# Kernel optimization log

Hardware: AMD Instinct MI355X
Metric: run time of the kernel (lower is better)

The kernel has to match this reference:

```python
import jax, jax.numpy as jnp
import numpy as np

WEIGHT = 1.0

# 3x3x3 discrete Laplacian stencil (6-connected, center -6), as in the torch module
_LAP_K = jnp.array(
    [[[0, 0, 0], [0, 1, 0], [0, 0, 0]],
     [[0, 1, 0], [1, -6, 1], [0, 1, 0]],
     [[0, 0, 0], [0, 1, 0], [0, 0, 0]]], dtype=jnp.float32)


def _abs_laplacian3d(x):
    """x: (N, D, H, W) -> |3D Laplacian(x)| with zero padding, same shape."""
    y = jax.lax.conv_general_dilated(
        x[:, None],              # (N, 1, D, H, W)
        _LAP_K[None, None],      # (1, 1, 3, 3, 3)
        window_strides=(1, 1, 1),
        padding=[(1, 1), (1, 1), (1, 1)])
    return jnp.abs(y[:, 0])


def setup_inputs() -> dict:
    key = jax.random.key(0)
    k1, k2 = jax.random.split(key)
    B, C, D, H, W = 2, 4, 64, 256, 256
    logits = jax.random.normal(k1, (B, C, D, H, W), dtype=jnp.float32)
    targets = jax.random.randint(k2, (B, D, H, W), 0, C)
    return {"logits": logits, "targets": targets}


def reference(logits, targets):
    B, C, D, H, W = logits.shape
    # softmax over class dim, drop background class 0 -> (B, C-1, D, H, W)
    probs = jax.nn.softmax(logits, axis=1)[:, 1:]
    # one-hot target masks for classes 1..C-1 -> (B, C-1, D, H, W)
    cls = jnp.arange(1, C)[None, :, None, None, None]
    tmask = (targets[:, None] == cls).astype(logits.dtype)
    # fused 3D Laplacian + abs over all (batch, class) pairs at once
    pred_b = _abs_laplacian3d(probs.reshape(B * (C - 1), D, H, W))
    targ_b = _abs_laplacian3d(tmask.reshape(B * (C - 1), D, H, W))
    # sum over classes of per-class MSE, divided by (C-1) == mean over everything
    return WEIGHT * jnp.mean((pred_b - targ_b) ** 2)
```

## Files before the change

### kernel.cpp

```cpp
#include <hip/hip_runtime.h>


#define CS   (1 << 22)
#define NTOT_INV (1.0f / 25165824.0f)
#define BIAS3 ((8 << 20) | (8 << 10) | 8)
#define BAR() asm volatile("s_waitcnt lgkmcnt(0)\n\ts_barrier" ::: "memory")

#define ISSUE(S, off)                                                        \
    S##0 = *(const float4*)(L + lBase + (off));                              \
    S##1 = *(const float4*)(L + lBase + (off) + CS);                         \
    S##2 = *(const float4*)(L + lBase + (off) + 2 * CS);                     \
    S##3 = *(const float4*)(L + lBase + (off) + 3 * CS);                     \
    S##t = *(const int4*)(T + tBase + (off));

__device__ __forceinline__ void smax1(float x0, float x1, float x2, float x3,
                                      float vm, float& p1, float& p2, float& p3) {
    float m  = fmaxf(fmaxf(x0, x1), fmaxf(x2, x3));
    float e0 = __expf(x0 - m);
    float e1 = __expf(x1 - m);
    float e2 = __expf(x2 - m);
    float e3 = __expf(x3 - m);
    float r  = vm * __builtin_amdgcn_rcpf(e0 + e1 + e2 + e3);
    p1 = e1 * r; p2 = e2 * r; p3 = e3 * r;
}

__device__ __forceinline__ int ohenc(int t, int msk) {
    int nz = (t > 0) ? 1 : 0;
    return (nz << (((t - 1) & 3) * 10)) & msk;
}

__global__ __launch_bounds__(512) void boundary_loss_kernel(
        const float* __restrict__ L,
        const int*   __restrict__ T,
        float*       __restrict__ out) {
    const int tid  = threadIdx.x;
    const int lane = tid & 63;
    const int th   = tid >> 6;
    int bi = blockIdx.x;
    const int dseg = bi & 7;  bi >>= 3;
    const int ht   = bi % 43;
    const int b    = bi / 43;

    const int   h   = ht * 6 + th - 1;
    const bool  hv  = ((unsigned)h < 256u);
    const int   hcl = min(max(h, 0), 255);
    const float vm  = hv ? 1.f : 0.f;
    const int   ohm = hv ? ~0 : 0;
    const bool  live = (th >= 1) && (th <= 6) && hv;
    const int   d0  = dseg << 3;

    const int rowoff = (hcl << 8) + (lane << 2);
    const int tBase  = b * CS + rowoff;
    const int lBase  = (b << 2) * CS + rowoff;

    __shared__ float P1[8][256], P2[8][256], P3[8][256];
    __shared__ int   OH[8][256];

    const int c0 = lane << 2;

    float4 c1, c2, c3; int4 coh;
    float4 a1, a2, a3; int4 aoh;
    float accv = 0.f;

    {
        const int   off  = (dseg > 0 ? d0 - 1 : 0) << 16;
        const float svm  = (dseg > 0) ? vm : 0.f;
        const int   sohm = (dseg > 0) ? ohm : 0;
        float4 q0, q1, q2, q3; int4 qt;
        ISSUE(q, off)
        smax1(q0.x, q1.x, q2.x, q3.x, svm, a1.x, a2.x, a3.x);
        smax1(q0.y, q1.y, q2.y, q3.y, svm, a1.y, a2.y, a3.y);
        smax1(q0.z, q1.z, q2.z, q3.z, svm, a1.z, a2.z, a3.z);
        smax1(q0.w, q1.w, q2.w, q3.w, svm, a1.w, a2.w, a3.w);
        aoh.x = ohenc(qt.x, sohm) + BIAS3; aoh.y = ohenc(qt.y, sohm) + BIAS3;
        aoh.z = ohenc(qt.z, sohm) + BIAS3; aoh.w = ohenc(qt.w, sohm) + BIAS3;
    }

    {
        const int off = d0 << 16;
        float4 q0, q1, q2, q3; int4 qt;
        ISSUE(q, off)
        smax1(q0.x, q1.x, q2.x, q3.x, vm, c1.x, c2.x, c3.x);
        smax1(q0.y, q1.y, q2.y, q3.y, vm, c1.y, c2.y, c3.y);
        smax1(q0.z, q1.z, q2.z, q3.z, vm, c1.z, c2.z, c3.z);
        smax1(q0.w, q1.w, q2.w, q3.w, vm, c1.w, c2.w, c3.w);
        coh.x = ohenc(qt.x, ohm); coh.y = ohenc(qt.y, ohm);
        coh.z = ohenc(qt.z, ohm); coh.w = ohenc(qt.w, ohm);
    }

    float4 A0, A1, A2, A3; int4 At;
    {
        const int off = (d0 + 1 < 64 ? d0 + 1 : 63) << 16;
        ISSUE(A, off)
    }

#pragma unroll
    for (int i = 0; i < 8; ++i) {
        float4 B0, B1, B2, B3; int4 Bt;
        B0 = B1 = B2 = B3 = make_float4(0.f, 0.f, 0.f, 0.f);
        Bt = make_int4(0, 0, 0, 0);
        if (i < 7) {
            const int off = (d0 + i + 2 < 64 ? d0 + i + 2 : 63) << 16;
            ISSUE(B, off)
        }

        BAR();
        *(float4*)&P1[th][c0] = c1;
        *(float4*)&P2[th][c0] = c2;
        *(float4*)&P3[th][c0] = c3;
        *(int4*)&OH[th][c0]   = coh;
        BAR();

        if (live) {
            float l1 = __shfl_up(c1.w, 1, 64);   float r1 = __shfl_down(c1.x, 1, 64);
            float l2 = __shfl_up(c2.w, 1, 64);   float r2 = __shfl_down(c2.x, 1, 64);
            float l3 = __shfl_up(c3.w, 1, 64);   float r3 = __shfl_down(c3.x, 1, 64);
            int   lo = __shfl_up(coh.w, 1, 64);  int   ro = __shfl_down(coh.x, 1, 64);
            if (lane == 0)  { l1 = l2 = l3 = 0.f; lo = 0; }
            if (lane == 63) { r1 = r2 = r3 = 0.f; ro = 0; }

            float4 u, v;
            u = *(float4*)&P1[th - 1][c0]; v = *(float4*)&P1[th + 1][c0];
            a1.x += u.x + v.x + l1   + c1.y - 6.f * c1.x;
            a1.y += u.y + v.y + c1.x + c1.z - 6.f * c1.y;
            a1.z += u.z + v.z + c1.y + c1.w - 6.f * c1.z;
            a1.w += u.w + v.w + c1.z + r1   - 6.f * c1.w;
            u = *(float4*)&P2[th - 1][c0]; v = *(float4*)&P2[th + 1][c0];
            a2.x += u.x + v.x + l2   + c2.y - 6.f * c2.x;
            a2.y += u.y + v.y + c2.x + c2.z - 6.f * c2.y;
            a2.z += u.z + v.z + c2.y + c2.w - 6.f * c2.z;
            a2.w += u.w + v.w + c2.z + r2   - 6.f * c2.w;
            u = *(float4*)&P3[th - 1][c0]; v = *(float4*)&P3[th + 1][c0];
            a3.x += u.x + v.x + l3   + c3.y - 6.f * c3.x;
            a3.y += u.y + v.y + c3.x + c3.z - 6.f * c3.y;
            a3.z += u.z + v.z + c3.y + c3.w - 6.f * c3.z;
            a3.w += u.w + v.w + c3.z + r3   - 6.f * c3.w;

            int4 iu = *(int4*)&OH[th - 1][c0];
            int4 id = *(int4*)&OH[th + 1][c0];
            aoh.x += iu.x + id.x + lo    + coh.y - 6 * coh.x;
            aoh.y += iu.y + id.y + coh.x + coh.z - 6 * coh.y;
            aoh.z += iu.z + id.z + coh.y + coh.w - 6 * coh.z;
            aoh.w += iu.w + id.w + coh.z + ro    - 6 * coh.w;
        }

        const int   dnA  = d0 + i + 1;
        const float vmn  = (dnA < 64) ? vm : 0.f;
        const int   ohmn = (dnA < 64) ? ohm : 0;
        float4 n1, n2, n3; int4 noh;
        smax1(A0.x, A1.x, A2.x, A3.x, vmn, n1.x, n2.x, n3.x);
        smax1(A0.y, A1.y, A2.y, A3.y, vmn, n1.y, n2.y, n3.y);
        smax1(A0.z, A1.z, A2.z, A3.z, vmn, n1.z, n2.z, n3.z);
        smax1(A0.w, A1.w, A2.w, A3.w, vmn, n1.w, n2.w, n3.w);
        noh.x = ohenc(At.x, ohmn); noh.y = ohenc(At.y, ohmn);
        noh.z = ohenc(At.z, ohmn); noh.w = ohenc(At.w, ohmn);

        if (live) {
            int t0 = aoh.x + noh.x, t1 = aoh.y + noh.y;
            int t2 = aoh.z + noh.z, t3 = aoh.w + noh.w;
            float lp, lt, df;
            lp = fabsf(a1.x + n1.x); lt = fabsf((float)((t0 & 1023) - 8));          df = lp - lt; accv = fmaf(df, df, accv);
            lp = fabsf(a2.x + n2.x); lt = fabsf((float)(((t0 >> 10) & 1023) - 8));  df = lp - lt; accv = fmaf(df, df, accv);
            lp = fabsf(a3.x + n3.x); lt = fabsf((float)(((t0 >> 20) & 1023) - 8));  df = lp - lt; accv = fmaf(df, df, accv);
            lp = fabsf(a1.y + n1.y); lt = fabsf((float)((t1 & 1023) - 8));          df = lp - lt; accv = fmaf(df, df, accv);
            lp = fabsf(a2.y + n2.y); lt = fabsf((float)(((t1 >> 10) & 1023) - 8));  df = lp - lt; accv = fmaf(df, df, accv);
            lp = fabsf(a3.y + n3.y); lt = fabsf((float)(((t1 >> 20) & 1023) - 8));  df = lp - lt; accv = fmaf(df, df, accv);
            lp = fabsf(a1.z + n1.z); lt = fabsf((float)((t2 & 1023) - 8));          df = lp - lt; accv = fmaf(df, df, accv);
            lp = fabsf(a2.z + n2.z); lt = fabsf((float)(((t2 >> 10) & 1023) - 8));  df = lp - lt; accv = fmaf(df, df, accv);
            lp = fabsf(a3.z + n3.z); lt = fabsf((float)(((t2 >> 20) & 1023) - 8));  df = lp - lt; accv = fmaf(df, df, accv);
            lp = fabsf(a1.w + n1.w); lt = fabsf((float)((t3 & 1023) - 8));          df = lp - lt; accv = fmaf(df, df, accv);
            lp = fabsf(a2.w + n2.w); lt = fabsf((float)(((t3 >> 10) & 1023) - 8));  df = lp - lt; accv = fmaf(df, df, accv);
            lp = fabsf(a3.w + n3.w); lt = fabsf((float)(((t3 >> 20) & 1023) - 8));  df = lp - lt; accv = fmaf(df, df, accv);
        }

        a1 = c1; a2 = c2; a3 = c3;
        aoh.x = coh.x + BIAS3; aoh.y = coh.y + BIAS3;
        aoh.z = coh.z + BIAS3; aoh.w = coh.w + BIAS3;
        c1 = n1; c2 = n2; c3 = n3; coh = noh;
        A0 = B0; A1 = B1; A2 = B2; A3 = B3; At = Bt;
    }

    for (int o = 32; o > 0; o >>= 1) accv += __shfl_down(accv, o, 64);
    __shared__ float wsum[8];
    if (lane == 0) wsum[th] = accv;
    __syncthreads();
    if (tid == 0) {
        float s = wsum[0] + wsum[1] + wsum[2] + wsum[3]
                + wsum[4] + wsum[5] + wsum[6] + wsum[7];
        atomicAdd(out, s * NTOT_INV);
    }
}

extern "C" void kernel_launch(void* const* d_in, const int* in_sizes, int n_in,
                              void* d_out, int out_size, void* d_ws, size_t ws_size,
                              hipStream_t stream) {
    const float* logits  = (const float*)d_in[0];
    const int*   targets = (const int*)d_in[1];
    float*       out     = (float*)d_out;

    hipMemsetAsync(out, 0, sizeof(float), stream);
    boundary_loss_kernel<<<688, 512, 0, stream>>>(logits, targets, out);
}
```

Before: 217.1 us.

## Split into a softmax-pack pass and a stencil pass over quantized probabilities

Adds a first kernel that computes the softmax once per voxel and packs three 10-bit quantized class probabilities plus the 2-bit target into one 32-bit word in the workspace. A second kernel runs the 3D Laplacian over this packed array, reading the up and down rows straight from global memory instead of sharing them through LDS and barriers. This removes the halo-row recomputation of softmax and the per-slice barriers of the fused kernel. In exchange it adds a 32 MB write and re-read of the intermediate, and an approximation error from 10-bit probability quantization. The fused kernel is kept as a fallback when the workspace is too small.

```diff
diff --git a/kernel.cpp b/kernel.cpp
--- a/kernel.cpp
+++ b/kernel.cpp
@@ -5,6 +5,180 @@
 #define NTOT_INV (1.0f / 25165824.0f)
 #define BIAS3 ((8 << 20) | (8 << 10) | 8)
 #define BAR() asm volatile("s_waitcnt lgkmcnt(0)\n\ts_barrier" ::: "memory")
+
+__device__ __forceinline__ unsigned enc1(float x0, float x1, float x2, float x3,
+                                         int t) {
+    float m  = fmaxf(fmaxf(x0, x1), fmaxf(x2, x3));
+    float e0 = __expf(x0 - m);
+    float e1 = __expf(x1 - m);
+    float e2 = __expf(x2 - m);
+    float e3 = __expf(x3 - m);
+    float r  = 1023.f * __builtin_amdgcn_rcpf(e0 + e1 + e2 + e3);
+    unsigned p1 = (unsigned)(e1 * r + 0.5f);
+    unsigned p2 = (unsigned)(e2 * r + 0.5f);
+    unsigned p3 = (unsigned)(e3 * r + 0.5f);
+    return p1 | (p2 << 10) | (p3 << 20) | ((unsigned)t << 30);
+}
+
+__global__ __launch_bounds__(256) void softmax_pack(
+        const float* __restrict__ L,
+        const int*   __restrict__ T,
+        unsigned*    __restrict__ P) {
+    const int t  = blockIdx.x * 256 + threadIdx.x;
+    const int v  = t << 2;
+    const int b  = v >> 22;
+    const int sp = v & (CS - 1);
+    const int lidx = ((b << 2) * CS) + sp;
+    float4 q0 = *(const float4*)(L + lidx);
+    float4 q1 = *(const float4*)(L + lidx + CS);
+    float4 q2 = *(const float4*)(L + lidx + 2 * CS);
+    float4 q3 = *(const float4*)(L + lidx + 3 * CS);
+    int4   qt = *(const int4*)(T + v);
+    uint4 o;
+    o.x = enc1(q0.x, q1.x, q2.x, q3.x, qt.x);
+    o.y = enc1(q0.y, q1.y, q2.y, q3.y, qt.y);
+    o.z = enc1(q0.z, q1.z, q2.z, q3.z, qt.z);
+    o.w = enc1(q0.w, q1.w, q2.w, q3.w, qt.w);
+    *(uint4*)(P + v) = o;
+}
+
+__device__ __forceinline__ void dec1(unsigned e, float sc, int om,
+                                     float& p1, float& p2, float& p3, int& oh) {
+    p1 = (float)(e & 1023u) * sc;
+    p2 = (float)((e >> 10) & 1023u) * sc;
+    p3 = (float)((e >> 20) & 1023u) * sc;
+    int tt = (int)(e >> 30);
+    oh = ((tt > 0 ? 1 : 0) << (((tt - 1) & 3) * 10)) & om;
+}
+
+#define DEC4(E, SC, OM, P1, P2, P3, OH)                                      \
+    dec1((E).x, SC, OM, (P1).x, (P2).x, (P3).x, (OH).x);                     \
+    dec1((E).y, SC, OM, (P1).y, (P2).y, (P3).y, (OH).y);                     \
+    dec1((E).z, SC, OM, (P1).z, (P2).z, (P3).z, (OH).z);                     \
+    dec1((E).w, SC, OM, (P1).w, (P2).w, (P3).w, (OH).w);
+
+__global__ __launch_bounds__(256) void stencil_pass(
+        const unsigned* __restrict__ P,
+        float*          __restrict__ out) {
+    const int tid  = threadIdx.x;
+    const int lane = tid & 63;
+    const int wv   = tid >> 6;
+    int bi = blockIdx.x;
+    const int dseg = bi & 7;  bi >>= 3;
+    const int h4   = bi & 63; bi >>= 6;
+    const int b    = bi;
+
+    const int h   = (h4 << 2) + wv;
+    const int hu  = (h > 0)   ? h - 1 : 0;
+    const int hdn = (h < 255) ? h + 1 : 255;
+    const float mc = 1.f / 1023.f;
+    const float mu = (h > 0)   ? mc : 0.f;
+    const float md = (h < 255) ? mc : 0.f;
+    const int   ou = (h > 0)   ? ~0 : 0;
+    const int   od = (h < 255) ? ~0 : 0;
+    const int d0   = dseg << 3;
+    const int baseB = b << 22;
+    const int col   = lane << 2;
+    const int rowC  = baseB + (h   << 8) + col;
+    const int rowU  = baseB + (hu  << 8) + col;
+    const int rowD  = baseB + (hdn << 8) + col;
+
+    float4 c1, c2, c3; int4 coh;
+    float4 a1, a2, a3; int4 aoh;
+    float accv = 0.f;
+
+    {
+        const int   dS = (dseg > 0) ? d0 - 1 : 0;
+        const float ms = (dseg > 0) ? mc : 0.f;
+        const int   os = (dseg > 0) ? ~0 : 0;
+        uint4 e = *(const uint4*)(P + rowC + (dS << 16));
+        DEC4(e, ms, os, a1, a2, a3, aoh)
+        aoh.x += BIAS3; aoh.y += BIAS3; aoh.z += BIAS3; aoh.w += BIAS3;
+    }
+    {
+        uint4 e = *(const uint4*)(P + rowC + (d0 << 16));
+        DEC4(e, mc, ~0, c1, c2, c3, coh)
+    }
+    uint4 An = *(const uint4*)(P + rowC + (min(d0 + 1, 63) << 16));
+    uint4 Au = *(const uint4*)(P + rowU + (d0 << 16));
+    uint4 Ad = *(const uint4*)(P + rowD + (d0 << 16));
+
+#pragma unroll
+    for (int i = 0; i < 8; ++i) {
+        const int d = d0 + i;
+        uint4 Bn = make_uint4(0, 0, 0, 0), Bu = Bn, Bd = Bn;
+        if (i < 7) {
+            Bn = *(const uint4*)(P + rowC + (min(d + 2, 63) << 16));
+            Bu = *(const uint4*)(P + rowU + ((d + 1) << 16));
+            Bd = *(const uint4*)(P + rowD + ((d + 1) << 16));
+        }
+
+        float4 u1, u2, u3; int4 uoh;
+        float4 v1, v2, v3; int4 voh;
+        DEC4(Au, mu, ou, u1, u2, u3, uoh)
+        DEC4(Ad, md, od, v1, v2, v3, voh)
+
+        float l1 = __shfl_up(c1.w, 1, 64);   float r1 = __shfl_down(c1.x, 1, 64);
+        float l2 = __shfl_up(c2.w, 1, 64);   float r2 = __shfl_down(c2.x, 1, 64);
+        float l3 = __shfl_up(c3.w, 1, 64);   float r3 = __shfl_down(c3.x, 1, 64);
+        int   lo = __shfl_up(coh.w, 1, 64);  int   ro = __shfl_down(coh.x, 1, 64);
+        if (lane == 0)  { l1 = l2 = l3 = 0.f; lo = 0; }
+        if (lane == 63) { r1 = r2 = r3 = 0.f; ro = 0; }
+
+        a1.x += u1.x + v1.x + l1   + c1.y - 6.f * c1.x;
+        a1.y += u1.y + v1.y + c1.x + c1.z - 6.f * c1.y;
+        a1.z += u1.z + v1.z + c1.y + c1.w - 6.f * c1.z;
+        a1.w += u1.w + v1.w + c1.z + r1   - 6.f * c1.w;
+        a2.x += u2.x + v2.x + l2   + c2.y - 6.f * c2.x;
+        a2.y += u2.y + v2.y + c2.x + c2.z - 6.f * c2.y;
+        a2.z += u2.z + v2.z + c2.y + c2.w - 6.f * c2.z;
+        a2.w += u2.w + v2.w + c2.z + r2   - 6.f * c2.w;
+        a3.x += u3.x + v3.x + l3   + c3.y - 6.f * c3.x;
+        a3.y += u3.y + v3.y + c3.x + c3.z - 6.f * c3.y;
+        a3.z += u3.z + v3.z + c3.y + c3.w - 6.f * c3.z;
+        a3.w += u3.w + v3.w + c3.z + r3   - 6.f * c3.w;
+        aoh.x += uoh.x + voh.x + lo    + coh.y - 6 * coh.x;
+        aoh.y += uoh.y + voh.y + coh.x + coh.z - 6 * coh.y;
+        aoh.z += uoh.z + voh.z + coh.y + coh.w - 6 * coh.z;
+        aoh.w += uoh.w + voh.w + coh.z + ro    - 6 * coh.w;
+
+        const float mn = (d + 1 < 64) ? mc : 0.f;
+        const int   on = (d + 1 < 64) ? ~0 : 0;
+        float4 n1, n2, n3; int4 noh;
+        DEC4(An, mn, on, n1, n2, n3, noh)
+
+        {
+            int t0 = aoh.x + noh.x, t1 = aoh.y + noh.y;
+            int t2 = aoh.z + noh.z, t3 = aoh.w + noh.w;
+            float lp, lt, df;
+            lp = fabsf(a1.x + n1.x); lt = fabsf((float)((t0 & 1023) - 8));          df = lp - lt; accv = fmaf(df, df, accv);
+            lp = fabsf(a2.x + n2.x); lt = fabsf((float)(((t0 >> 10) & 1023) - 8));  df = lp - lt; accv = fmaf(df, df, accv);
+            lp = fabsf(a3.x + n3.x); lt = fabsf((float)(((t0 >> 20) & 1023) - 8));  df = lp - lt; accv = fmaf(df, df, accv);
+            lp = fabsf(a1.y + n1.y); lt = fabsf((float)((t1 & 1023) - 8));          df = lp - lt; accv = fmaf(df, df, accv);
+            lp = fabsf(a2.y + n2.y); lt = fabsf((float)(((t1 >> 10) & 1023) - 8));  df = lp - lt; accv = fmaf(df, df, accv);
+            lp = fabsf(a3.y + n3.y); lt = fabsf((float)(((t1 >> 20) & 1023) - 8));  df = lp - lt; accv = fmaf(df, df, accv);
+            lp = fabsf(a1.z + n1.z); lt = fabsf((float)((t2 & 1023) - 8));          df = lp - lt; accv = fmaf(df, df, accv);
+            lp = fabsf(a2.z + n2.z); lt = fabsf((float)(((t2 >> 10) & 1023) - 8));  df = lp - lt; accv = fmaf(df, df, accv);
+            lp = fabsf(a3.z + n3.z); lt = fabsf((float)(((t2 >> 20) & 1023) - 8));  df = lp - lt; accv = fmaf(df, df, accv);
+            lp = fabsf(a1.w + n1.w); lt = fabsf((float)((t3 & 1023) - 8));          df = lp - lt; accv = fmaf(df, df, accv);
+            lp = fabsf(a2.w + n2.w); lt = fabsf((float)(((t3 >> 10) & 1023) - 8));  df = lp - lt; accv = fmaf(df, df, accv);
+            lp = fabsf(a3.w + n3.w); lt = fabsf((float)(((t3 >> 20) & 1023) - 8));  df = lp - lt; accv = fmaf(df, df, accv);
+        }
+
+        a1 = c1; a2 = c2; a3 = c3;
+        aoh.x = coh.x + BIAS3; aoh.y = coh.y + BIAS3;
+        aoh.z = coh.z + BIAS3; aoh.w = coh.w + BIAS3;
+        c1 = n1; c2 = n2; c3 = n3; coh = noh;
+        An = Bn; Au = Bu; Ad = Bd;
+    }
+
+    for (int o = 32; o > 0; o >>= 1) accv += __shfl_down(accv, o, 64);
+    __shared__ float wsum[4];
+    if (lane == 0) wsum[wv] = accv;
+    __syncthreads();
+    if (tid == 0)
+        atomicAdd(out, (wsum[0] + wsum[1] + wsum[2] + wsum[3]) * NTOT_INV);
+}
 
 #define ISSUE(S, off)                                                        \
     S##0 = *(const float4*)(L + lBase + (off));                              \
@@ -55,7 +229,6 @@
 
     __shared__ float P1[8][256], P2[8][256], P3[8][256];
     __shared__ int   OH[8][256];
-
     const int c0 = lane << 2;
 
     float4 c1, c2, c3; int4 coh;
@@ -75,7 +248,6 @@
         aoh.x = ohenc(qt.x, sohm) + BIAS3; aoh.y = ohenc(qt.y, sohm) + BIAS3;
         aoh.z = ohenc(qt.z, sohm) + BIAS3; aoh.w = ohenc(qt.w, sohm) + BIAS3;
     }
-
     {
         const int off = d0 << 16;
         float4 q0, q1, q2, q3; int4 qt;
@@ -87,13 +259,11 @@
         coh.x = ohenc(qt.x, ohm); coh.y = ohenc(qt.y, ohm);
         coh.z = ohenc(qt.z, ohm); coh.w = ohenc(qt.w, ohm);
     }
-
     float4 A0, A1, A2, A3; int4 At;
     {
         const int off = (d0 + 1 < 64 ? d0 + 1 : 63) << 16;
         ISSUE(A, off)
     }
-
 #pragma unroll
     for (int i = 0; i < 8; ++i) {
         float4 B0, B1, B2, B3; int4 Bt;
@@ -103,14 +273,12 @@
             const int off = (d0 + i + 2 < 64 ? d0 + i + 2 : 63) << 16;
             ISSUE(B, off)
         }
-
         BAR();
         *(float4*)&P1[th][c0] = c1;
         *(float4*)&P2[th][c0] = c2;
         *(float4*)&P3[th][c0] = c3;
         *(int4*)&OH[th][c0]   = coh;
         BAR();
-
         if (live) {
             float l1 = __shfl_up(c1.w, 1, 64);   float r1 = __shfl_down(c1.x, 1, 64);
             float l2 = __shfl_up(c2.w, 1, 64);   float r2 = __shfl_down(c2.x, 1, 64);
@@ -118,7 +286,6 @@
             int   lo = __shfl_up(coh.w, 1, 64);  int   ro = __shfl_down(coh.x, 1, 64);
             if (lane == 0)  { l1 = l2 = l3 = 0.f; lo = 0; }
             if (lane == 63) { r1 = r2 = r3 = 0.f; ro = 0; }
-
             float4 u, v;
             u = *(float4*)&P1[th - 1][c0]; v = *(float4*)&P1[th + 1][c0];
             a1.x += u.x + v.x + l1   + c1.y - 6.f * c1.x;
@@ -135,7 +302,6 @@
             a3.y += u.y + v.y + c3.x + c3.z - 6.f * c3.y;
             a3.z += u.z + v.z + c3.y + c3.w - 6.f * c3.z;
             a3.w += u.w + v.w + c3.z + r3   - 6.f * c3.w;
-
             int4 iu = *(int4*)&OH[th - 1][c0];
             int4 id = *(int4*)&OH[th + 1][c0];
             aoh.x += iu.x + id.x + lo    + coh.y - 6 * coh.x;
@@ -143,7 +309,6 @@
             aoh.z += iu.z + id.z + coh.y + coh.w - 6 * coh.z;
             aoh.w += iu.w + id.w + coh.z + ro    - 6 * coh.w;
         }
-
         const int   dnA  = d0 + i + 1;
         const float vmn  = (dnA < 64) ? vm : 0.f;
         const int   ohmn = (dnA < 64) ? ohm : 0;
@@ -154,7 +319,6 @@
         smax1(A0.w, A1.w, A2.w, A3.w, vmn, n1.w, n2.w, n3.w);
         noh.x = ohenc(At.x, ohmn); noh.y = ohenc(At.y, ohmn);
         noh.z = ohenc(At.z, ohmn); noh.w = ohenc(At.w, ohmn);
-
         if (live) {
             int t0 = aoh.x + noh.x, t1 = aoh.y + noh.y;
             int t2 = aoh.z + noh.z, t3 = aoh.w + noh.w;
@@ -172,14 +336,12 @@
             lp = fabsf(a2.w + n2.w); lt = fabsf((float)(((t3 >> 10) & 1023) - 8));  df = lp - lt; accv = fmaf(df, df, accv);
             lp = fabsf(a3.w + n3.w); lt = fabsf((float)(((t3 >> 20) & 1023) - 8));  df = lp - lt; accv = fmaf(df, df, accv);
         }
-
         a1 = c1; a2 = c2; a3 = c3;
         aoh.x = coh.x + BIAS3; aoh.y = coh.y + BIAS3;
         aoh.z = coh.z + BIAS3; aoh.w = coh.w + BIAS3;
         c1 = n1; c2 = n2; c3 = n3; coh = noh;
         A0 = B0; A1 = B1; A2 = B2; A3 = B3; At = Bt;
     }
-
     for (int o = 32; o > 0; o >>= 1) accv += __shfl_down(accv, o, 64);
     __shared__ float wsum[8];
     if (lane == 0) wsum[th] = accv;
@@ -199,5 +361,12 @@
     float*       out     = (float*)d_out;
 
     hipMemsetAsync(out, 0, sizeof(float), stream);
-    boundary_loss_kernel<<<688, 512, 0, stream>>>(logits, targets, out);
-}
+
+    if (ws_size >= (size_t)(1u << 25)) {
+        unsigned* P = (unsigned*)d_ws;
+        softmax_pack<<<8192, 256, 0, stream>>>(logits, targets, P);
+        stencil_pass<<<1024, 256, 0, stream>>>(P, out);
+    } else {
+        boundary_loss_kernel<<<688, 512, 0, stream>>>(logits, targets, out);
+    }
+}
```

Result: slower. 238.0 us (+9.7%).
